# Optimization experiments

Hardware: AMD Instinct MI355X
Metric: run time of the kernel (lower is better)

Reference implementation:

```python
import jax, jax.numpy as jnp
import numpy as np

H = 8          # num_heads
BM = 128       # block_size_m
BN = 128       # block_size_n
EPS = 1e-6
CAUSAL = True  # config.causal


def setup_inputs() -> dict:
    key = jax.random.key(0)
    ks = jax.random.split(key, 5)
    B, N, D = 1, 2048, 512
    s = 1.0 / np.sqrt(D)
    # small-scale x so projected points mostly stay inside the Poincare ball
    x = jax.random.normal(ks[0], (B, N, D), jnp.float32) * 0.05
    return {
        'x': x,
        'c': jnp.ones((1,), jnp.float32),
        'Wq': jax.random.normal(ks[1], (D, D), jnp.float32) * s,
        'bq': jnp.zeros((D,), jnp.float32),
        'Wk': jax.random.normal(ks[2], (D, D), jnp.float32) * s,
        'bk': jnp.zeros((D,), jnp.float32),
        'Wv': jax.random.normal(ks[3], (D, D), jnp.float32) * s,
        'bv': jnp.zeros((D,), jnp.float32),
        'Wo': jax.random.normal(ks[4], (D, D), jnp.float32) * s,
        'bo': jnp.zeros((D,), jnp.float32),
    }


def reference(x, c, Wq, bq, Wk, bk, Wv, bv, Wo, bo):
    B, N, D = x.shape
    Dh = D // H
    cc = jnp.clip(jnp.abs(c), 1e-6)            # (1,) learned curvature, abs+clamp as in torch
    sqrt_c = jnp.sqrt(jnp.clip(cc, EPS))

    def proj(W, b):
        return (x @ W + b).reshape(B, N, H, Dh).transpose(0, 2, 1, 3)  # (B,H,N,Dh)

    q, k, v = proj(Wq, bq), proj(Wk, bk), proj(Wv, bv)

    # Poincare distance: ||q-k||^2 expanded via norms (same math as explicit diff tensor)
    qn = (q ** 2).sum(-1)                      # (B,H,N)
    kn = (k ** 2).sum(-1)                      # (B,H,N)
    qk = jnp.einsum('bhmd,bhnd->bhmn', q, k)   # (B,H,N,N)
    diff_sq = jnp.clip(qn[..., :, None] + kn[..., None, :] - 2.0 * qk, 0.0)
    denom = jnp.clip((1.0 - cc * qn)[..., :, None] * (1.0 - cc * kn)[..., None, :], EPS)
    arg = jnp.clip(1.0 + 2.0 * cc * diff_sq / denom, 1.0 + EPS)
    scores = -jnp.arccosh(arg) / sqrt_c        # (B,H,N,N)

    # block-wise softmax: each 128x128 block subtracts ITS OWN max (faithful to torch code,
    # which omits cross-block max rescaling), then exp-sums are accumulated across blocks.
    nbm, nbn = N // BM, N // BN
    s = scores.reshape(B, H, nbm, BM, nbn, BN)
    row = jnp.arange(nbm)[:, None]
    col = jnp.arange(nbn)[None, :]
    skip = (col > row) if CAUSAL else jnp.zeros((nbm, nbn), bool)   # skipped upper blocks
    diag = (col == row) if CAUSAL else jnp.zeros((nbm, nbn), bool)
    tri = jnp.triu(jnp.ones((BM, BN), bool), 1)
    mask = skip[:, None, :, None] | (diag[:, None, :, None] & tri[None, :, None, :])  # (nbm,BM,nbn,BN)

    s_masked = jnp.where(mask, -jnp.inf, s)
    bmax = s_masked.max(axis=-1, keepdims=True)                      # per-block-row max over BN
    bmax = jnp.where(jnp.isfinite(bmax), bmax, 0.0)                  # skipped blocks -> safe
    e = jnp.where(mask, 0.0, jnp.exp(s - bmax))                      # (B,H,nbm,BM,nbn,BN)

    normalizer = jnp.clip(e.sum(axis=(4, 5)).reshape(B, H, N), EPS)  # (B,H,N)
    vb = v.reshape(B, H, nbn, BN, Dh)
    out = jnp.einsum('bhrmcn,bhcnd->bhrmd', e, vb).reshape(B, H, N, Dh)
    out = out / normalizer[..., None]
    out = out.transpose(0, 2, 1, 3).reshape(B, N, D)
    return out @ Wo + bo
```

## Files before the change

### kernel.cpp

```cpp
#include <hip/hip_runtime.h>
#include <math.h>

#define D_MODEL 512
#define NHEADS  8
#define NSEQ    2048
#define NBLK    16
#define NCHUNK  72
#define EPSF    1e-6f
#define WPLANE  262144

typedef _Float16 v8h __attribute__((ext_vector_type(8)));
typedef _Float16 v4h __attribute__((ext_vector_type(4)));
typedef float    v4f __attribute__((ext_vector_type(4)));

static __device__ __forceinline__ v4f mfma16h(v8h a, v8h b, v4f c) {
  return __builtin_amdgcn_mfma_f32_16x16x32_f16(a, b, c, 0, 0, 0);
}

__global__ __launch_bounds__(256) void prep_w(const float* __restrict__ W0,
                                              const float* __restrict__ W1,
                                              const float* __restrict__ W2,
                                              const float* __restrict__ W3,
                                              _Float16* __restrict__ Wth) {
  __shared__ float T[64][68];
  const int z = blockIdx.z;
  const float* W = (z == 0) ? W0 : (z == 1) ? W1 : (z == 2) ? W2 : W3;
  const int kb = blockIdx.x * 64;
  const int nb = blockIdx.y * 64;
  const int tid = threadIdx.x;
#pragma unroll
  for (int l = 0; l < 4; ++l) {
    int f = tid + l * 256;
    int row = f >> 4, c4 = f & 15;
    float4 v = *reinterpret_cast<const float4*>(&W[(size_t)(kb + row) * D_MODEL + nb + c4 * 4]);
    T[c4 * 4 + 0][row] = v.x; T[c4 * 4 + 1][row] = v.y;
    T[c4 * 4 + 2][row] = v.z; T[c4 * 4 + 3][row] = v.w;
  }
  __syncthreads();
  _Float16* oh = Wth + (size_t)z * WPLANE;
#pragma unroll
  for (int l = 0; l < 4; ++l) {
    int f = tid + l * 256;
    int n_ = f >> 4, k4 = f & 15;
    v4h h4;
    h4[0] = (_Float16)T[n_][k4 * 4 + 0];
    h4[1] = (_Float16)T[n_][k4 * 4 + 1];
    h4[2] = (_Float16)T[n_][k4 * 4 + 2];
    h4[3] = (_Float16)T[n_][k4 * 4 + 3];
    *reinterpret_cast<v4h*>(&oh[(size_t)(nb + n_) * D_MODEL + kb + k4 * 4]) = h4;
  }
}

__global__ __launch_bounds__(256) void qkv_gemm(
    const float* __restrict__ x, const _Float16* __restrict__ Wth,
    const float* __restrict__ bq, const float* __restrict__ bk,
    const float* __restrict__ bv,
    _Float16* __restrict__ Qp, _Float16* __restrict__ Kp,
    _Float16* __restrict__ Vp,
    float* __restrict__ Qn_, float* __restrict__ Kn_) {
  __shared__ _Float16 Ah[128][40], Bh[128][40];
  const int z = blockIdx.z;
  const _Float16* Bt = Wth + (size_t)z * WPLANE;
  const float* bias = (z == 0) ? bq : (z == 1) ? bk : bv;
  _Float16* outp = (z == 0) ? Qp : (z == 1) ? Kp : Vp;

  const int bx = blockIdx.x, by = blockIdx.y;
  const int tid = threadIdx.x;
  const int wid = tid >> 6, lane = tid & 63;
  const int wr = wid >> 1, wc = wid & 1;
  const int g = lane >> 4, lx = lane & 15;

  v4f acc[4][4];
#pragma unroll
  for (int i = 0; i < 4; ++i)
#pragma unroll
    for (int j = 0; j < 4; ++j) acc[i][j] = v4f{0.f, 0.f, 0.f, 0.f};

  for (int k0 = 0; k0 < 16; ++k0) {
    __syncthreads();
#pragma unroll
    for (int l = 0; l < 4; ++l) {
      int f = tid + l * 256;
      int row = f >> 3, c4 = f & 7;
      float4 a = *reinterpret_cast<const float4*>(&x[(size_t)(by * 128 + row) * D_MODEL + k0 * 32 + c4 * 4]);
      Ah[row][c4 * 4 + 0] = (_Float16)a.x;
      Ah[row][c4 * 4 + 1] = (_Float16)a.y;
      Ah[row][c4 * 4 + 2] = (_Float16)a.z;
      Ah[row][c4 * 4 + 3] = (_Float16)a.w;
    }
#pragma unroll
    for (int l = 0; l < 2; ++l) {
      int f = tid + l * 256;
      int row = f >> 2, c8 = f & 3;
      *reinterpret_cast<uint4*>(&Bh[row][c8 * 8]) =
          *reinterpret_cast<const uint4*>(&Bt[(size_t)(bx * 128 + row) * D_MODEL + k0 * 32 + c8 * 8]);
    }
    __syncthreads();
    v8h ah[4], bh[4];
#pragma unroll
    for (int i = 0; i < 4; ++i) {
      ah[i] = *reinterpret_cast<const v8h*>(&Ah[wr * 64 + i * 16 + lx][g * 8]);
      bh[i] = *reinterpret_cast<const v8h*>(&Bh[wc * 64 + i * 16 + lx][g * 8]);
    }
#pragma unroll
    for (int i = 0; i < 4; ++i)
#pragma unroll
      for (int j = 0; j < 4; ++j)
        acc[i][j] = mfma16h(ah[i], bh[j], acc[i][j]);
  }

  float np[4][4];
#pragma unroll
  for (int i = 0; i < 4; ++i)
#pragma unroll
    for (int r = 0; r < 4; ++r) np[i][r] = 0.f;

#pragma unroll
  for (int j = 0; j < 4; ++j) {
    const int col = bx * 128 + wc * 64 + j * 16 + lx;
    const float bj = bias[col];
#pragma unroll
    for (int i = 0; i < 4; ++i)
#pragma unroll
      for (int r = 0; r < 4; ++r) {
        const int row = by * 128 + wr * 64 + i * 16 + g * 4 + r;
        float v = acc[i][j][r] + bj;
        _Float16 hv = (_Float16)v;
        outp[(size_t)row * D_MODEL + col] = hv;
        float vr = (float)hv;
        np[i][r] = fmaf(vr, vr, np[i][r]);
      }
  }
  if (z < 2) {
    float* Nout = (z == 0) ? Qn_ : Kn_;
    const int hh = bx * 2 + wc;
#pragma unroll
    for (int i = 0; i < 4; ++i)
#pragma unroll
      for (int r = 0; r < 4; ++r) {
        float s = np[i][r];
        s += __shfl_xor(s, 1, 64);
        s += __shfl_xor(s, 2, 64);
        s += __shfl_xor(s, 4, 64);
        s += __shfl_xor(s, 8, 64);
        if (lx == 0)
          Nout[hh * NSEQ + by * 128 + wr * 64 + i * 16 + g * 4 + r] = s;
      }
  }
}

__global__ __launch_bounds__(256) void vt_prep(const ushort* __restrict__ Vb,
                                               ushort* __restrict__ Vtb) {
  __shared__ ushort T[64][72];
  const int nb = blockIdx.x * 64;
  const int h  = blockIdx.y;
  const int tid = threadIdx.x;
#pragma unroll
  for (int l = 0; l < 2; ++l) {
    int f = tid + l * 256;
    int row = f >> 3, c8 = f & 7;
    uint4 w = *reinterpret_cast<const uint4*>(&Vb[(size_t)(nb + row) * D_MODEL + h * 64 + c8 * 8]);
    const ushort* p = reinterpret_cast<const ushort*>(&w);
#pragma unroll
    for (int j = 0; j < 8; ++j) T[c8 * 8 + j][row] = p[j];
  }
  __syncthreads();
#pragma unroll
  for (int l = 0; l < 2; ++l) {
    int f = tid + l * 256;
    int d = f >> 3, n8 = f & 7;
    *reinterpret_cast<uint4*>(&Vtb[(size_t)(h * 64 + d) * NSEQ + nb + n8 * 8]) =
        *reinterpret_cast<const uint4*>(&T[d][n8 * 8]);
  }
}

__global__ __launch_bounds__(512, 4) void attn(
    const _Float16* __restrict__ Qp, const _Float16* __restrict__ Kp,
    const _Float16* __restrict__ Vtb, const float* __restrict__ Qn,
    const float* __restrict__ Kn, const float* __restrict__ cptr,
    float* __restrict__ Opart, float* __restrict__ Npart)
{
  __shared__ _Float16 Khs[128][68];
  __shared__ _Float16 Vs[64][136];
  __shared__ _Float16 Es[128][136];
  __shared__ float kns[128];

  const int bid = blockIdx.x;
  const int h    = bid & 7;
  const int pid2 = bid >> 3;
  int m = 0, base = 0;
  while (base + (m / 2 + 1) <= pid2) { base += m / 2 + 1; ++m; }
  const int c  = pid2 - base;
  const int n0 = 2 * c;
  const int n1 = (n0 + 1 < m) ? n0 + 1 : m;

  const int tid  = threadIdx.x;
  const int w    = tid >> 6;
  const int lane = tid & 63;
  const int g = lane >> 4, lx = lane & 15;

  const float cc = fmaxf(fabsf(cptr[0]), 1e-6f);
  const float is = rsqrtf(cc);
  const bool is_one = (cc == 1.0f);
  const float two_cc = 2.f * cc;

  const int krow = tid >> 3, kc8 = tid & 7;
  const int vrow = tid >> 4, vc8 = tid & 15;

  const _Float16* Kgh = Kp + h * 64;
  const _Float16* Vgh = Vtb + (size_t)(h * 64) * NSEQ;

  uint4 kpre0, kpre1, vpre0, vpre1;
  float knp = 0.f;
  {
    const _Float16* Kg = Kgh + (size_t)(n0 * 128) * D_MODEL;
    kpre0 = *reinterpret_cast<const uint4*>(&Kg[(size_t)krow * D_MODEL + kc8 * 8]);
    kpre1 = *reinterpret_cast<const uint4*>(&Kg[(size_t)(krow + 64) * D_MODEL + kc8 * 8]);
    vpre0 = *reinterpret_cast<const uint4*>(&Vgh[(size_t)vrow * NSEQ + n0 * 128 + vc8 * 8]);
    vpre1 = *reinterpret_cast<const uint4*>(&Vgh[(size_t)(vrow + 32) * NSEQ + n0 * 128 + vc8 * 8]);
    if (tid < 128) knp = Kn[h * NSEQ + n0 * 128 + tid];
  }
  *reinterpret_cast<uint4*>(&Khs[krow][kc8 * 8]) = kpre0;
  *reinterpret_cast<uint4*>(&Khs[krow + 64][kc8 * 8]) = kpre1;
  *reinterpret_cast<uint4*>(&Vs[vrow][vc8 * 8]) = vpre0;
  *reinterpret_cast<uint4*>(&Vs[vrow + 32][vc8 * 8]) = vpre1;
  if (tid < 128) kns[tid] = knp;
  __syncthreads();

  v8h aQ[2];
  {
    const size_t qoff = (size_t)(m * 128 + 16 * w + lx) * D_MODEL + h * 64 + g * 8;
    aQ[0] = *reinterpret_cast<const v8h*>(&Qp[qoff]);
    aQ[1] = *reinterpret_cast<const v8h*>(&Qp[qoff + 32]);
  }
  float qnr[4], qar[4];
#pragma unroll
  for (int r = 0; r < 4; ++r) {
    qnr[r] = Qn[h * NSEQ + m * 128 + 16 * w + g * 4 + r];
    qar[r] = fmaf(-cc, qnr[r], 1.f);
  }

  v4f o_acc[4];
#pragma unroll
  for (int td = 0; td < 4; ++td) o_acc[td] = v4f{0.f, 0.f, 0.f, 0.f};
  float nrm[4] = {0.f, 0.f, 0.f, 0.f};

  for (int n = n0; n <= n1; ++n) {
    const bool more = (n < n1);
    if (more) {
      const _Float16* Kg = Kgh + (size_t)((n + 1) * 128) * D_MODEL;
      kpre0 = *reinterpret_cast<const uint4*>(&Kg[(size_t)krow * D_MODEL + kc8 * 8]);
      kpre1 = *reinterpret_cast<const uint4*>(&Kg[(size_t)(krow + 64) * D_MODEL + kc8 * 8]);
      vpre0 = *reinterpret_cast<const uint4*>(&Vgh[(size_t)vrow * NSEQ + (n + 1) * 128 + vc8 * 8]);
      vpre1 = *reinterpret_cast<const uint4*>(&Vgh[(size_t)(vrow + 32) * NSEQ + (n + 1) * 128 + vc8 * 8]);
      if (tid < 128) knp = Kn[h * NSEQ + (n + 1) * 128 + tid];
    }

    v4f acc[8];
#pragma unroll
    for (int tn = 0; tn < 8; ++tn) {
      v8h b0 = *reinterpret_cast<const v8h*>(&Khs[tn * 16 + lx][g * 8]);
      v8h b1 = *reinterpret_cast<const v8h*>(&Khs[tn * 16 + lx][g * 8 + 32]);
      v4f a = v4f{0.f, 0.f, 0.f, 0.f};
      a = mfma16h(aQ[0], b0, a);
      a = mfma16h(aQ[1], b1, a);
      acc[tn] = a;
    }

    const bool diag = (n == m);
#pragma unroll
    for (int tn = 0; tn < 8; ++tn) {
      const int col = tn * 16 + lx;
      const float knc = kns[col];
      const float kac = fmaf(-cc, knc, 1.f);
#pragma unroll
      for (int r = 0; r < 4; ++r) {
        const int rowl = 16 * w + g * 4 + r;
        float dsq = fmaxf(fmaf(-2.f, acc[tn][r], qnr[r] + knc), 0.f);
        float den = fmaxf(qar[r] * kac, EPSF);
        float t = fmaxf(two_cc * dsq * __builtin_amdgcn_rcpf(den), EPSF);
        float u = 1.f + t + __builtin_amdgcn_sqrtf(t * (t + 2.f));
        if (diag && col > rowl) u = __builtin_inff();
        acc[tn][r] = u;
      }
    }

    if (is_one) {
      float umin[4] = {__builtin_inff(), __builtin_inff(), __builtin_inff(), __builtin_inff()};
#pragma unroll
      for (int tn = 0; tn < 8; ++tn)
#pragma unroll
        for (int r = 0; r < 4; ++r) umin[r] = fminf(umin[r], acc[tn][r]);
#pragma unroll
      for (int d = 1; d < 16; d <<= 1)
#pragma unroll
        for (int r = 0; r < 4; ++r) umin[r] = fminf(umin[r], __shfl_xor(umin[r], d, 64));
#pragma unroll
      for (int tn = 0; tn < 8; ++tn)
#pragma unroll
        for (int r = 0; r < 4; ++r) {
          float e = umin[r] * __builtin_amdgcn_rcpf(acc[tn][r]);
          nrm[r] += e;
          Es[16 * w + g * 4 + r][tn * 16 + lx] = (_Float16)e;
        }
    } else {
      float smax[4] = {-__builtin_inff(), -__builtin_inff(), -__builtin_inff(), -__builtin_inff()};
#pragma unroll
      for (int tn = 0; tn < 8; ++tn)
#pragma unroll
        for (int r = 0; r < 4; ++r) {
          float s = -__logf(acc[tn][r]) * is;
          acc[tn][r] = s;
          smax[r] = fmaxf(smax[r], s);
        }
#pragma unroll
      for (int d = 1; d < 16; d <<= 1)
#pragma unroll
        for (int r = 0; r < 4; ++r) smax[r] = fmaxf(smax[r], __shfl_xor(smax[r], d, 64));
#pragma unroll
      for (int tn = 0; tn < 8; ++tn)
#pragma unroll
        for (int r = 0; r < 4; ++r) {
          float e = __expf(acc[tn][r] - smax[r]);
          nrm[r] += e;
          Es[16 * w + g * 4 + r][tn * 16 + lx] = (_Float16)e;
        }
    }
    asm volatile("s_waitcnt lgkmcnt(0)" ::: "memory");
    __builtin_amdgcn_sched_barrier(0);

#pragma unroll
    for (int ks = 0; ks < 4; ++ks) {
      v8h ea = *reinterpret_cast<const v8h*>(&Es[16 * w + lx][ks * 32 + g * 8]);
#pragma unroll
      for (int td = 0; td < 4; ++td) {
        v8h vb = *reinterpret_cast<const v8h*>(&Vs[td * 16 + lx][ks * 32 + g * 8]);
        o_acc[td] = mfma16h(ea, vb, o_acc[td]);
      }
    }

    if (more) {
      __syncthreads();
      *reinterpret_cast<uint4*>(&Khs[krow][kc8 * 8]) = kpre0;
      *reinterpret_cast<uint4*>(&Khs[krow + 64][kc8 * 8]) = kpre1;
      *reinterpret_cast<uint4*>(&Vs[vrow][vc8 * 8]) = vpre0;
      *reinterpret_cast<uint4*>(&Vs[vrow + 32][vc8 * 8]) = vpre1;
      if (tid < 128) kns[tid] = knp;
      __syncthreads();
    }
  }

#pragma unroll
  for (int d = 1; d < 16; d <<= 1)
#pragma unroll
    for (int r = 0; r < 4; ++r) nrm[r] += __shfl_xor(nrm[r], d, 64);

  float* Op = Opart + ((size_t)h * NCHUNK + pid2) * (128 * 64);
#pragma unroll
  for (int td = 0; td < 4; ++td)
#pragma unroll
    for (int r = 0; r < 4; ++r)
      Op[(size_t)(16 * w + g * 4 + r) * 64 + td * 16 + lx] = o_acc[td][r];
  if (lx == 0) {
#pragma unroll
    for (int r = 0; r < 4; ++r)
      Npart[((size_t)h * NCHUNK + pid2) * 128 + 16 * w + g * 4 + r] = nrm[r];
  }
}

__global__ __launch_bounds__(256) void reduce_o(const float* __restrict__ Opart,
                                                const float* __restrict__ Npart,
                                                _Float16* __restrict__ Of) {
  const int mq = blockIdx.x;
  const int mm = mq >> 2;
  const int rq = (mq & 3) * 32;
  const int h  = blockIdx.y;
  const int tid = threadIdx.x;
  int base = 0;
  for (int k = 0; k < mm; ++k) base += k / 2 + 1;
  const int nch = mm / 2 + 1;

  __shared__ float innorm[32];
  if (tid < 32) {
    float s = 0.f;
    for (int cI = 0; cI < nch; ++cI)
      s += Npart[((size_t)h * NCHUNK + base + cI) * 128 + rq + tid];
    innorm[tid] = 1.f / fmaxf(s, EPSF);
  }
  __syncthreads();
#pragma unroll
  for (int l = 0; l < 2; ++l) {
    int f = tid + l * 256;
    int r = f >> 4, c4 = f & 15;
    float4 s = {0.f, 0.f, 0.f, 0.f};
    for (int cI = 0; cI < nch; ++cI) {
      const float4 p = *reinterpret_cast<const float4*>(
          &Opart[((size_t)h * NCHUNK + base + cI) * 8192 + (size_t)(rq + r) * 64 + c4 * 4]);
      s.x += p.x; s.y += p.y; s.z += p.z; s.w += p.w;
    }
    float inv = innorm[r];
    v4h o4;
    o4[0] = (_Float16)(s.x * inv); o4[1] = (_Float16)(s.y * inv);
    o4[2] = (_Float16)(s.z * inv); o4[3] = (_Float16)(s.w * inv);
    *reinterpret_cast<v4h*>(
        &Of[(size_t)(mm * 128 + rq + r) * D_MODEL + h * 64 + c4 * 4]) = o4;
  }
}

__global__ __launch_bounds__(256) void o_gemm(const _Float16* __restrict__ Of,
                                              const _Float16* __restrict__ Wth,
                                              const float* __restrict__ bo,
                                              float* __restrict__ out) {
  __shared__ _Float16 As[64][40], Bs[64][40];
  const _Float16* Bt = Wth + (size_t)3 * WPLANE;
  const int bx = blockIdx.x, by = blockIdx.y;
  const int tid = threadIdx.x;
  const int wid = tid >> 6, lane = tid & 63;
  const int wr = wid >> 1, wc = wid & 1;
  const int g = lane >> 4, lx = lane & 15;

  v4f acc[2][2];
#pragma unroll
  for (int i = 0; i < 2; ++i)
#pragma unroll
    for (int j = 0; j < 2; ++j) acc[i][j] = v4f{0.f, 0.f, 0.f, 0.f};

  const int srow = tid >> 2, sc8 = tid & 3;
  for (int k0 = 0; k0 < 16; ++k0) {
    __syncthreads();
    *reinterpret_cast<uint4*>(&As[srow][sc8 * 8]) =
        *reinterpret_cast<const uint4*>(&Of[(size_t)(by * 64 + srow) * D_MODEL + k0 * 32 + sc8 * 8]);
    *reinterpret_cast<uint4*>(&Bs[srow][sc8 * 8]) =
        *reinterpret_cast<const uint4*>(&Bt[(size_t)(bx * 64 + srow) * D_MODEL + k0 * 32 + sc8 * 8]);
    __syncthreads();
    v8h ah[2][2], bh[2][2];
#pragma unroll
    for (int i = 0; i < 2; ++i) {
      ah[i][0] = *reinterpret_cast<const v8h*>(&As[wr * 32 + i * 16 + lx][g * 8]);
      bh[i][0] = *reinterpret_cast<const v8h*>(&Bs[wc * 32 + i * 16 + lx][g * 8]);
    }
#pragma unroll
    for (int i = 0; i < 2; ++i)
#pragma unroll
      for (int j = 0; j < 2; ++j)
        acc[i][j] = mfma16h(ah[i][0], bh[j][0], acc[i][j]);
  }
#pragma unroll
  for (int j = 0; j < 2; ++j) {
    const int col = bx * 64 + wc * 32 + j * 16 + lx;
    const float bj = bo[col];
#pragma unroll
    for (int i = 0; i < 2; ++i)
#pragma unroll
      for (int r = 0; r < 4; ++r) {
        const int row = by * 64 + wr * 32 + i * 16 + g * 4 + r;
        out[(size_t)row * D_MODEL + col] = acc[i][j][r] + bj;
      }
  }
}

extern "C" void kernel_launch(void* const* d_in, const int* in_sizes, int n_in,
                              void* d_out, int out_size, void* d_ws, size_t ws_size,
                              hipStream_t stream) {
  (void)in_sizes; (void)n_in; (void)out_size; (void)ws_size;
  const float* x  = (const float*)d_in[0];
  const float* cfg= (const float*)d_in[1];
  const float* Wq = (const float*)d_in[2];
  const float* bq = (const float*)d_in[3];
  const float* Wk = (const float*)d_in[4];
  const float* bk = (const float*)d_in[5];
  const float* Wv = (const float*)d_in[6];
  const float* bv = (const float*)d_in[7];
  const float* Wo = (const float*)d_in[8];
  const float* bo = (const float*)d_in[9];
  float* out = (float*)d_out;

  char* p = (char*)d_ws;
  const size_t PL = (size_t)NSEQ * D_MODEL * sizeof(_Float16);
  _Float16* Wth = (_Float16*)p;        p += 4 * (size_t)WPLANE * sizeof(_Float16);
  _Float16* Qp  = (_Float16*)p;        p += PL;
  _Float16* Kp  = (_Float16*)p;        p += PL;
  _Float16* Vp  = (_Float16*)p;        p += PL;
  _Float16* Vtb = (_Float16*)p;        p += PL;
  _Float16* Of  = (_Float16*)p;        p += PL;
  float*  Qn  = (float*)p;             p += (size_t)NHEADS * NSEQ * sizeof(float);
  float*  Kn  = (float*)p;             p += (size_t)NHEADS * NSEQ * sizeof(float);
  float*  Opart = (float*)p;           p += (size_t)NHEADS * NCHUNK * 8192 * sizeof(float);
  float*  Npart = (float*)p;

  prep_w<<<dim3(8, 8, 4), 256, 0, stream>>>(Wq, Wk, Wv, Wo, Wth);
  qkv_gemm<<<dim3(4, 16, 3), 256, 0, stream>>>(x, Wth, bq, bk, bv,
                                               Qp, Kp, Vp, Qn, Kn);
  vt_prep<<<dim3(32, 8), 256, 0, stream>>>((const ushort*)Vp, (ushort*)Vtb);
  attn<<<dim3(NCHUNK * NHEADS), 512, 0, stream>>>(Qp, Kp, Vtb, Qn, Kn, cfg,
                                                  Opart, Npart);
  reduce_o<<<dim3(64, NHEADS), 256, 0, stream>>>(Opart, Npart, Of);
  o_gemm<<<dim3(8, 32), 256, 0, stream>>>(Of, Wth, bo, out);
}
```

Baseline: 86.67 us.

## Split attention P·V into halves with per-wave E tiles, setprio, higher occupancy

Shrinks the shared E buffer to a per-wave 16x64 tile and splits the exp/write and P·V MFMA phase into two halves. This lets each wave interleave its softmax math with MFMAs and cuts LDS use so occupancy can rise; launch bounds move from 4 to 6 blocks. It also raises wave priority around the MFMA loops, pads the V tile differently, and writes partial outputs with nontemporal stores. Tighter register limits from the higher launch bound risk spills.

```diff
diff --git a/kernel.cpp b/kernel.cpp
--- a/kernel.cpp
+++ b/kernel.cpp
@@ -174,15 +174,15 @@
   }
 }
 
-__global__ __launch_bounds__(512, 4) void attn(
+__global__ __launch_bounds__(512, 6) void attn(
     const _Float16* __restrict__ Qp, const _Float16* __restrict__ Kp,
     const _Float16* __restrict__ Vtb, const float* __restrict__ Qn,
     const float* __restrict__ Kn, const float* __restrict__ cptr,
     float* __restrict__ Opart, float* __restrict__ Npart)
 {
   __shared__ _Float16 Khs[128][68];
-  __shared__ _Float16 Vs[64][136];
-  __shared__ _Float16 Es[128][136];
+  __shared__ _Float16 Vs[64][140];
+  __shared__ _Float16 Es[8][16][68];
   __shared__ float kns[128];
 
   const int bid = blockIdx.x;
@@ -257,6 +257,7 @@
     }
 
     v4f acc[8];
+    __builtin_amdgcn_s_setprio(1);
 #pragma unroll
     for (int tn = 0; tn < 8; ++tn) {
       v8h b0 = *reinterpret_cast<const v8h*>(&Khs[tn * 16 + lx][g * 8]);
@@ -266,6 +267,7 @@
       a = mfma16h(aQ[1], b1, a);
       acc[tn] = a;
     }
+    __builtin_amdgcn_s_setprio(0);
 
     const bool diag = (n == m);
 #pragma unroll
@@ -285,58 +287,62 @@
       }
     }
 
+    float mred[4];
     if (is_one) {
-      float umin[4] = {__builtin_inff(), __builtin_inff(), __builtin_inff(), __builtin_inff()};
+#pragma unroll
+      for (int r = 0; r < 4; ++r) mred[r] = __builtin_inff();
 #pragma unroll
       for (int tn = 0; tn < 8; ++tn)
 #pragma unroll
-        for (int r = 0; r < 4; ++r) umin[r] = fminf(umin[r], acc[tn][r]);
+        for (int r = 0; r < 4; ++r) mred[r] = fminf(mred[r], acc[tn][r]);
 #pragma unroll
       for (int d = 1; d < 16; d <<= 1)
 #pragma unroll
-        for (int r = 0; r < 4; ++r) umin[r] = fminf(umin[r], __shfl_xor(umin[r], d, 64));
-#pragma unroll
-      for (int tn = 0; tn < 8; ++tn)
-#pragma unroll
-        for (int r = 0; r < 4; ++r) {
-          float e = umin[r] * __builtin_amdgcn_rcpf(acc[tn][r]);
-          nrm[r] += e;
-          Es[16 * w + g * 4 + r][tn * 16 + lx] = (_Float16)e;
-        }
+        for (int r = 0; r < 4; ++r) mred[r] = fminf(mred[r], __shfl_xor(mred[r], d, 64));
     } else {
-      float smax[4] = {-__builtin_inff(), -__builtin_inff(), -__builtin_inff(), -__builtin_inff()};
+#pragma unroll
+      for (int r = 0; r < 4; ++r) mred[r] = -__builtin_inff();
 #pragma unroll
       for (int tn = 0; tn < 8; ++tn)
 #pragma unroll
         for (int r = 0; r < 4; ++r) {
           float s = -__logf(acc[tn][r]) * is;
           acc[tn][r] = s;
-          smax[r] = fmaxf(smax[r], s);
+          mred[r] = fmaxf(mred[r], s);
         }
 #pragma unroll
       for (int d = 1; d < 16; d <<= 1)
 #pragma unroll
-        for (int r = 0; r < 4; ++r) smax[r] = fmaxf(smax[r], __shfl_xor(smax[r], d, 64));
-#pragma unroll
-      for (int tn = 0; tn < 8; ++tn)
+        for (int r = 0; r < 4; ++r) mred[r] = fmaxf(mred[r], __shfl_xor(mred[r], d, 64));
+    }
+
+#pragma unroll
+    for (int half = 0; half < 2; ++half) {
+#pragma unroll
+      for (int tn2 = 0; tn2 < 4; ++tn2) {
+        const int tn = half * 4 + tn2;
 #pragma unroll
         for (int r = 0; r < 4; ++r) {
-          float e = __expf(acc[tn][r] - smax[r]);
+          float e = is_one ? mred[r] * __builtin_amdgcn_rcpf(acc[tn][r])
+                           : __expf(acc[tn][r] - mred[r]);
           nrm[r] += e;
-          Es[16 * w + g * 4 + r][tn * 16 + lx] = (_Float16)e;
+          Es[w][g * 4 + r][tn2 * 16 + lx] = (_Float16)e;
         }
-    }
-    asm volatile("s_waitcnt lgkmcnt(0)" ::: "memory");
-    __builtin_amdgcn_sched_barrier(0);
-
-#pragma unroll
-    for (int ks = 0; ks < 4; ++ks) {
-      v8h ea = *reinterpret_cast<const v8h*>(&Es[16 * w + lx][ks * 32 + g * 8]);
-#pragma unroll
-      for (int td = 0; td < 4; ++td) {
-        v8h vb = *reinterpret_cast<const v8h*>(&Vs[td * 16 + lx][ks * 32 + g * 8]);
-        o_acc[td] = mfma16h(ea, vb, o_acc[td]);
       }
+      asm volatile("s_waitcnt lgkmcnt(0)" ::: "memory");
+      __builtin_amdgcn_sched_barrier(0);
+      __builtin_amdgcn_s_setprio(1);
+#pragma unroll
+      for (int ks2 = 0; ks2 < 2; ++ks2) {
+        const int ks = half * 2 + ks2;
+        v8h ea = *reinterpret_cast<const v8h*>(&Es[w][lx][ks2 * 32 + g * 8]);
+#pragma unroll
+        for (int td = 0; td < 4; ++td) {
+          v8h vb = *reinterpret_cast<const v8h*>(&Vs[td * 16 + lx][ks * 32 + g * 8]);
+          o_acc[td] = mfma16h(ea, vb, o_acc[td]);
+        }
+      }
+      __builtin_amdgcn_s_setprio(0);
     }
 
     if (more) {
@@ -360,11 +366,13 @@
   for (int td = 0; td < 4; ++td)
 #pragma unroll
     for (int r = 0; r < 4; ++r)
-      Op[(size_t)(16 * w + g * 4 + r) * 64 + td * 16 + lx] = o_acc[td][r];
+      __builtin_nontemporal_store(o_acc[td][r],
+          &Op[(size_t)(16 * w + g * 4 + r) * 64 + td * 16 + lx]);
   if (lx == 0) {
 #pragma unroll
     for (int r = 0; r < 4; ++r)
-      Npart[((size_t)h * NCHUNK + pid2) * 128 + 16 * w + g * 4 + r] = nrm[r];
+      __builtin_nontemporal_store(nrm[r],
+          &Npart[((size_t)h * NCHUNK + pid2) * 128 + 16 * w + g * 4 + r]);
   }
 }
 
@@ -433,17 +441,17 @@
     *reinterpret_cast<uint4*>(&Bs[srow][sc8 * 8]) =
         *reinterpret_cast<const uint4*>(&Bt[(size_t)(bx * 64 + srow) * D_MODEL + k0 * 32 + sc8 * 8]);
     __syncthreads();
-    v8h ah[2][2], bh[2][2];
+    v8h ah[2], bh[2];
 #pragma unroll
     for (int i = 0; i < 2; ++i) {
-      ah[i][0] = *reinterpret_cast<const v8h*>(&As[wr * 32 + i * 16 + lx][g * 8]);
-      bh[i][0] = *reinterpret_cast<const v8h*>(&Bs[wc * 32 + i * 16 + lx][g * 8]);
+      ah[i] = *reinterpret_cast<const v8h*>(&As[wr * 32 + i * 16 + lx][g * 8]);
+      bh[i] = *reinterpret_cast<const v8h*>(&Bs[wc * 32 + i * 16 + lx][g * 8]);
     }
 #pragma unroll
     for (int i = 0; i < 2; ++i)
 #pragma unroll
       for (int j = 0; j < 2; ++j)
-        acc[i][j] = mfma16h(ah[i][0], bh[j][0], acc[i][j]);
+        acc[i][j] = mfma16h(ah[i], bh[j], acc[i][j]);
   }
 #pragma unroll
   for (int j = 0; j < 2; ++j) {
```

Measured after the change: 108.1 us. 1.25x slower.
